# Optimization experiments

Hardware: AMD Instinct MI355X
Metric: run time of the kernel (lower is better)

The kernel has to match this reference:

```python
import jax, jax.numpy as jnp
import numpy as np

D_MODEL = 1024
NUM_HEADS = 16
NUM_KV_HEADS = 4
HEAD_DIM = D_MODEL // NUM_HEADS  # 64
KV_DIM = HEAD_DIM * NUM_KV_HEADS  # 256
B, N = 2, 2048


def setup_inputs() -> dict:
    key = jax.random.key(0)
    ks = jax.random.split(key, 7)
    std = 1.0 / np.sqrt(D_MODEL)
    return {
        "x": jax.random.normal(ks[0], (B, N, D_MODEL), dtype=jnp.float32),
        "cos": jax.random.uniform(ks[1], (N, HEAD_DIM // 2), dtype=jnp.float32),
        "sin": jax.random.uniform(ks[2], (N, HEAD_DIM // 2), dtype=jnp.float32),
        "Wq": jax.random.normal(ks[3], (D_MODEL, D_MODEL), dtype=jnp.float32) * std,
        "Wk": jax.random.normal(ks[4], (D_MODEL, KV_DIM), dtype=jnp.float32) * std,
        "Wv": jax.random.normal(ks[5], (D_MODEL, KV_DIM), dtype=jnp.float32) * std,
        "Wo": jax.random.normal(ks[6], (D_MODEL, D_MODEL), dtype=jnp.float32) * std,
    }


def _rope(t, cos, sin):
    # t: [B, H, N, head_dim]; cos/sin: [N, head_dim//2]
    t1, t2 = t[..., ::2], t[..., 1::2]
    c = cos[None, None]
    s = sin[None, None]
    # NOTE: halves are concatenated (not re-interleaved), faithful to source.
    return jnp.concatenate([t1 * c - t2 * s, t1 * s + t2 * c], axis=-1)


def reference(x, cos, sin, Wq, Wk, Wv, Wo):
    b, n, d = x.shape
    scale = HEAD_DIM ** -0.5
    q = (x @ Wq).reshape(b, n, NUM_HEADS, HEAD_DIM).transpose(0, 2, 1, 3)
    k = (x @ Wk).reshape(b, n, NUM_KV_HEADS, HEAD_DIM).transpose(0, 2, 1, 3)
    v = (x @ Wv).reshape(b, n, NUM_KV_HEADS, HEAD_DIM).transpose(0, 2, 1, 3)
    q = _rope(q, cos, sin)
    k = _rope(k, cos, sin)
    num_rep = NUM_HEADS // NUM_KV_HEADS
    k = jnp.repeat(k, num_rep, axis=1)  # [b, H, n, hd]
    v = jnp.repeat(v, num_rep, axis=1)
    attn = jnp.einsum("bhqd,bhkd->bhqk", q, k) * scale
    attn = jax.nn.softmax(attn, axis=-1)
    out = jnp.einsum("bhqk,bhkd->bhqd", attn, v)
    out = out.transpose(0, 2, 1, 3).reshape(b, n, d)
    return out @ Wo
```

## Files before the change

### kernel.cpp

```cpp
#include <hip/hip_runtime.h>
#include <math.h>

#define D_MODEL 1024
#define NHEADS  16
#define NKV     4
#define HDIM    64
#define KVDIM   256
#define BB      2
#define NN      2048
#define MROWS   (BB*NN)
#define QKVN    1536
#define NTASK   (MROWS*NHEADS)
#define NSPLIT  2
#define KVBLK   128
#define NTILE   ((NN/NSPLIT)/KVBLK)

typedef unsigned short ushort_t;
typedef unsigned int uint_t;
typedef float    f32x4 __attribute__((ext_vector_type(4)));
typedef _Float16 h16x8 __attribute__((ext_vector_type(8)));
typedef _Float16 h16x4 __attribute__((ext_vector_type(4)));
typedef __fp16   fp16x2 __attribute__((ext_vector_type(2)));

#define MFMAH(A,B,C)  __builtin_amdgcn_mfma_f32_16x16x32_f16((A),(B),(C),0,0,0)
#define MFMA16(A,B,C) __builtin_amdgcn_mfma_f32_16x16x16f16((A),(B),(C),0,0,0)
#define EXP2(x) __builtin_amdgcn_exp2f(x)

#define GLDS(gp, lp) __builtin_amdgcn_global_load_lds( \
    (const __attribute__((address_space(1))) void*)(gp), \
    (__attribute__((address_space(3))) void*)(lp), 16, 0, 0)

__device__ __forceinline__ ushort_t f2h(float f) {
    _Float16 h = (_Float16)f;
    return *(ushort_t*)&h;
}
__device__ __forceinline__ float h2f(ushort_t u) {
    return (float)(*(const _Float16*)&u);
}
__device__ __forceinline__ uint_t pk2h(float a, float b) {
    fp16x2 v = __builtin_amdgcn_cvt_pkrtz(a, b);
    return *(uint_t*)&v;
}

__global__ __launch_bounds__(256)
void prep_kernel(const float* __restrict__ x, const float* __restrict__ Wq,
                 const float* __restrict__ Wk, const float* __restrict__ Wv,
                 const float* __restrict__ Wo, ushort_t* __restrict__ xb,
                 ushort_t* __restrict__ WqkvT, ushort_t* __restrict__ WoT)
{
    __shared__ float T[32][33];
    int blk = blockIdx.x;
    if (blk < 4096) {
        const int i = blk * 256 + threadIdx.x;
        float4 v = ((const float4*)x)[i];
        uint2 o;
        o.x = pk2h(v.x, v.y);
        o.y = pk2h(v.z, v.w);
        ((uint2*)xb)[i] = o;
        return;
    }
    blk -= 4096;
    const float* src; ushort_t* dst; int N, bx, by;
    if (blk < 1024)      { src = Wq; dst = WqkvT;                            N = D_MODEL; bx = blk & 31; by = blk >> 5; }
    else if (blk < 1280) { blk -= 1024; src = Wk; dst = WqkvT + (size_t)1024 * D_MODEL; N = KVDIM; bx = blk & 7; by = blk >> 3; }
    else if (blk < 1536) { blk -= 1280; src = Wv; dst = WqkvT + (size_t)1280 * D_MODEL; N = KVDIM; bx = blk & 7; by = blk >> 3; }
    else                 { blk -= 1536; src = Wo; dst = WoT;                 N = D_MODEL; bx = blk & 31; by = blk >> 5; }
    const int tx = threadIdx.x & 31, ty = threadIdx.x >> 5;
    const int n0 = bx * 32, k0 = by * 32;
#pragma unroll
    for (int i = 0; i < 4; i++)
        T[ty + i * 8][tx] = src[(size_t)(k0 + ty + i * 8) * N + n0 + tx];
    __syncthreads();
#pragma unroll
    for (int i = 0; i < 4; i++)
        dst[(size_t)(n0 + ty + i * 8) * D_MODEL + k0 + tx] = f2h(T[tx][ty + i * 8]);
}

#define NKW (MROWS*NKV*32)
#define NKBLK (NKW / 256)
__global__ __launch_bounds__(256)
void ropevt_kernel(const ushort_t* __restrict__ QKVh, const float* __restrict__ Cos,
                   const float* __restrict__ Sin, ushort_t* __restrict__ Kb,
                   ushort_t* __restrict__ Vt)
{
    __shared__ ushort_t T[32][34];
    if (blockIdx.x >= NKBLK) {
        const int blk2 = blockIdx.x - NKBLK;
        const int bx = blk2 & 63, by = (blk2 >> 6) & 7, b = blk2 >> 9;
        const int tx = threadIdx.x & 31, ty = threadIdx.x >> 5;
        const int n0 = bx * 32, d0 = by * 32;
#pragma unroll
        for (int i = 0; i < 4; i++)
            T[ty + i * 8][tx] =
                QKVh[(size_t)(b * NN + n0 + ty + i * 8) * QKVN + 1280 + d0 + tx];
        __syncthreads();
#pragma unroll
        for (int i = 0; i < 4; i++)
            Vt[(size_t)(b * 256 + d0 + ty + i * 8) * NN + n0 + tx] = T[tx][ty + i * 8];
        return;
    }
    const int i2 = blockIdx.x * 256 + threadIdx.x;
    const int row = i2 >> 7, rem = i2 & 127;
    const int h = rem >> 5, j = rem & 31;
    const int b = row >> 11, n = row & (NN - 1);
    const uint_t pr = *(const uint_t*)&QKVh[(size_t)row * QKVN + 1024 + h * 64 + 2 * j];
    const float e = h2f((ushort_t)pr), o = h2f((ushort_t)(pr >> 16));
    const float c = Cos[n * 32 + j], s = Sin[n * 32 + j];
    ushort_t* dst = Kb + ((size_t)(b * 4 + h) * NN + n) * 64;
    dst[j]      = f2h(e * c - o * s);
    dst[j + 32] = f2h(e * s + o * c);
}

__global__ __launch_bounds__(256)
void gemm_qkv(const ushort_t* __restrict__ A, const ushort_t* __restrict__ Bt,
              ushort_t* __restrict__ C, int M, int N, int K)
{
    __shared__ ushort_t As[2][128 * 32];
    __shared__ ushort_t Bs[2][64 * 32];

    const int tid  = threadIdx.x;
    const int wave = tid >> 6, lane = tid & 63;
    const int quad = lane >> 4, l16 = lane & 15;
    const int rowBase = blockIdx.y * 128, colBase = blockIdx.x * 64;
    const int wm = (wave >> 1) * 64, wn = (wave & 1) * 32;

    f32x4 acc[4][2];
    const f32x4 zz = {0.f, 0.f, 0.f, 0.f};
#pragma unroll
    for (int i = 0; i < 4; i++)
#pragma unroll
        for (int j = 0; j < 2; j++) acc[i][j] = zz;

    const int sr = wave * 32 + (lane >> 2);
    const int sc = ((lane & 3) ^ ((lane >> 3) & 3)) * 8;
    const ushort_t* Ag0 = A + (size_t)(rowBase + sr) * K + sc;
    const ushort_t* Ag1 = A + (size_t)(rowBase + sr + 16) * K + sc;
    const int segA0 = (wave * 2 + 0) * 512, segA1 = (wave * 2 + 1) * 512;
    const int br = wave * 16 + (lane >> 2);
    const ushort_t* Bg0 = Bt + (size_t)(colBase + br) * K + sc;
    const int segB = wave * 512;

    const int fcol = (quad ^ ((l16 >> 1) & 3)) * 8;

    GLDS(Ag0, &As[0][segA0]);
    GLDS(Ag1, &As[0][segA1]);
    GLDS(Bg0, &Bs[0][segB]);

    for (int k0 = 0; k0 < K; k0 += 32) {
        const int cur = (k0 >> 5) & 1, nxt = cur ^ 1;
        __syncthreads();
        if (k0 + 32 < K) {
            GLDS(Ag0 + k0 + 32, &As[nxt][segA0]);
            GLDS(Ag1 + k0 + 32, &As[nxt][segA1]);
            GLDS(Bg0 + k0 + 32, &Bs[nxt][segB]);
        }

        h16x8 af[4], bf[2];
#pragma unroll
        for (int mt = 0; mt < 4; mt++)
            af[mt] = *(const h16x8*)&As[cur][(wm + mt * 16 + l16) * 32 + fcol];
#pragma unroll
        for (int nt = 0; nt < 2; nt++)
            bf[nt] = *(const h16x8*)&Bs[cur][(wn + nt * 16 + l16) * 32 + fcol];
#pragma unroll
        for (int mt = 0; mt < 4; mt++)
#pragma unroll
            for (int nt = 0; nt < 2; nt++)
                acc[mt][nt] = MFMAH(af[mt], bf[nt], acc[mt][nt]);
    }

#pragma unroll
    for (int mt = 0; mt < 4; mt++)
#pragma unroll
        for (int nt = 0; nt < 2; nt++) {
            const int row = rowBase + wm + mt * 16 + quad * 4;
            const int col = colBase + wn + nt * 16 + l16;
#pragma unroll
            for (int r = 0; r < 4; r++)
                C[(size_t)(row + r) * N + col] = f2h(acc[mt][nt][r]);
        }
}

__global__ __launch_bounds__(256)
void attn_mfma(const ushort_t* __restrict__ QKVh, const float* __restrict__ Cos,
               const float* __restrict__ Sin, const ushort_t* __restrict__ Kb,
               const ushort_t* __restrict__ Vt, ushort_t* __restrict__ Pnum,
               float* __restrict__ Pl)
{
    const int qt = blockIdx.x, h = blockIdx.y;
    const int b = blockIdx.z >> 1, chunk = blockIdx.z & 1;
    const int kvh = h >> 2;
    const int tid = threadIdx.x;
    const int wave = tid >> 6, lane = tid & 63;
    const int quad = lane >> 4, l16 = lane & 15;

    __shared__ ushort_t Ks[128][72];
    __shared__ ushort_t Vs[64][136];

    const int row0 = qt * 256 + wave * 64;
    const float SC = 0.125f * 1.44269504f;

    h16x8 qf[4][2];
#pragma unroll
    for (int mt = 0; mt < 4; mt++) {
        const int n = row0 + mt * 16 + l16;
        const uint_t* pr =
            (const uint_t*)(QKVh + (size_t)(b * NN + n) * QKVN + h * 64) + quad * 8;
        uint4 pa = *(const uint4*)pr;
        uint4 pc = *(const uint4*)(pr + 4);
        const uint_t pk[8] = {pa.x, pa.y, pa.z, pa.w, pc.x, pc.y, pc.z, pc.w};
        const float4 c0 = *(const float4*)&Cos[(size_t)n * 32 + quad * 8];
        const float4 c1 = *(const float4*)&Cos[(size_t)n * 32 + quad * 8 + 4];
        const float4 s0 = *(const float4*)&Sin[(size_t)n * 32 + quad * 8];
        const float4 s1 = *(const float4*)&Sin[(size_t)n * 32 + quad * 8 + 4];
        const float cc[8] = {c0.x, c0.y, c0.z, c0.w, c1.x, c1.y, c1.z, c1.w};
        const float ss[8] = {s0.x, s0.y, s0.z, s0.w, s1.x, s1.y, s1.z, s1.w};
#pragma unroll
        for (int i = 0; i < 8; i++) {
            const float e = h2f((ushort_t)pk[i]);
            const float o = h2f((ushort_t)(pk[i] >> 16));
            qf[mt][0][i] = (_Float16)((e * cc[i] - o * ss[i]) * SC);
            qf[mt][1][i] = (_Float16)((e * ss[i] + o * cc[i]) * SC);
        }
    }

    h16x4 ones;
#pragma unroll
    for (int i = 0; i < 4; i++) ones[i] = (_Float16)1.0f;

    const ushort_t* kbase = Kb + (size_t)(b * 4 + kvh) * NN * 64;
    const ushort_t* vbase = Vt + (size_t)(b * 256 + kvh * 64) * NN;
    const int key_lo = chunk * (NN / NSPLIT);
    const int rot = (qt + ((h & 3) << 2)) & (NTILE - 1);

    const int srow = tid >> 2, sseg = (tid & 3) * 8;
    const ushort_t* kp_lane = kbase + (size_t)srow * 64 + sseg;
    const ushort_t* vp_lane = vbase + (size_t)srow * NN + sseg;

    const f32x4 zz = {0.f, 0.f, 0.f, 0.f};
    f32x4 o[4][4];
#pragma unroll
    for (int mt = 0; mt < 4; mt++)
#pragma unroll
        for (int dt = 0; dt < 4; dt++) o[mt][dt] = zz;
    f32x4 lsum[4];
#pragma unroll
    for (int mt = 0; mt < 4; mt++) lsum[mt] = zz;

    const int key0 = key_lo + rot * KVBLK;
    uint4 kreg0 = *(const uint4*)(kp_lane + (size_t)key0 * 64);
    uint4 kreg1 = *(const uint4*)(kp_lane + (size_t)key0 * 64 + 32);
    uint4 kreg2 = *(const uint4*)(kp_lane + (size_t)(key0 + 64) * 64);
    uint4 kreg3 = *(const uint4*)(kp_lane + (size_t)(key0 + 64) * 64 + 32);
    uint4 vreg0 = *(const uint4*)(vp_lane + key0);
    uint4 vreg1 = *(const uint4*)(vp_lane + key0 + 32);
    uint4 vreg2 = *(const uint4*)(vp_lane + key0 + 64);
    uint4 vreg3 = *(const uint4*)(vp_lane + key0 + 96);

    for (int t = 0; t < NTILE; t++) {
        __syncthreads();
        *(uint4*)&Ks[srow][sseg]           = kreg0;
        *(uint4*)&Ks[srow][sseg + 32]      = kreg1;
        *(uint4*)&Ks[srow + 64][sseg]      = kreg2;
        *(uint4*)&Ks[srow + 64][sseg + 32] = kreg3;
        *(uint4*)&Vs[srow][sseg]           = vreg0;
        *(uint4*)&Vs[srow][sseg + 32]      = vreg1;
        *(uint4*)&Vs[srow][sseg + 64]      = vreg2;
        *(uint4*)&Vs[srow][sseg + 96]      = vreg3;
        __syncthreads();

        if (t < NTILE - 1) {
            const int kn = key_lo + ((rot + t + 1) & (NTILE - 1)) * KVBLK;
            kreg0 = *(const uint4*)(kp_lane + (size_t)kn * 64);
            kreg1 = *(const uint4*)(kp_lane + (size_t)kn * 64 + 32);
            kreg2 = *(const uint4*)(kp_lane + (size_t)(kn + 64) * 64);
            kreg3 = *(const uint4*)(kp_lane + (size_t)(kn + 64) * 64 + 32);
            vreg0 = *(const uint4*)(vp_lane + kn);
            vreg1 = *(const uint4*)(vp_lane + kn + 32);
            vreg2 = *(const uint4*)(vp_lane + kn + 64);
            vreg3 = *(const uint4*)(vp_lane + kn + 96);
        }

#pragma unroll
        for (int kt = 0; kt < 8; kt++) {
            h16x8 kf0 = *(const h16x8*)&Ks[kt * 16 + l16][quad * 8];
            h16x8 kf1 = *(const h16x8*)&Ks[kt * 16 + l16][32 + quad * 8];
            h16x4 va[4];
#pragma unroll
            for (int dt = 0; dt < 4; dt++)
                va[dt] = *(const h16x4*)&Vs[dt * 16 + l16][kt * 16 + quad * 4];

            uint2 pb[4];
#pragma unroll
            for (int mt = 0; mt < 4; mt++) {
                f32x4 st = MFMAH(kf0, qf[mt][0], zz);
                st = MFMAH(kf1, qf[mt][1], st);
                pb[mt].x = pk2h(EXP2(st[0]), EXP2(st[1]));
                pb[mt].y = pk2h(EXP2(st[2]), EXP2(st[3]));
            }
#pragma unroll
            for (int mt = 0; mt < 4; mt++) {
                const h16x4 pbv = *(const h16x4*)&pb[mt];
#pragma unroll
                for (int dt = 0; dt < 4; dt++)
                    o[mt][dt] = MFMA16(va[dt], pbv, o[mt][dt]);
                lsum[mt] = MFMA16(ones, pbv, lsum[mt]);
            }
        }
    }

    const size_t task0 = (size_t)(b * 16 + h) * NN + row0;
    ushort_t* np = Pnum + ((size_t)chunk * NTASK + task0) * 64;
#pragma unroll
    for (int mt = 0; mt < 4; mt++) {
        const float lt = lsum[mt][0];
        const float inv = 1.0f / lt;
#pragma unroll
        for (int dt = 0; dt < 4; dt++) {
            f32x4 v = o[mt][dt];
            uint2 pk;
            pk.x = pk2h(v[0] * inv, v[1] * inv);
            pk.y = pk2h(v[2] * inv, v[3] * inv);
            *(uint2*)&np[(size_t)(mt * 16 + l16) * 64 + dt * 16 + quad * 4] = pk;
        }
        if (quad == 0)
            Pl[(size_t)chunk * NTASK + task0 + mt * 16 + l16] = lt;
    }
}

__global__ __launch_bounds__(256)
void gemm_wo(const ushort_t* __restrict__ Pnum, const float* __restrict__ Pl,
             const ushort_t* __restrict__ WoT, float* __restrict__ C)
{
    __shared__ ushort_t As[2][128 * 40];
    __shared__ ushort_t Bs[2][64 * 32];

    const int tid  = threadIdx.x;
    const int wave = tid >> 6, lane = tid & 63;
    const int quad = lane >> 4, l16 = lane & 15;
    const int rowBase = blockIdx.y * 128, colBase = blockIdx.x * 64;
    const int wm = (wave >> 1) * 64, wn = (wave & 1) * 32;

    f32x4 acc[4][2];
    const f32x4 zz = {0.f, 0.f, 0.f, 0.f};
#pragma unroll
    for (int i = 0; i < 4; i++)
#pragma unroll
        for (int j = 0; j < 2; j++) acc[i][j] = zz;

    const int r0 = tid >> 2;
    const int c8 = (tid & 3) * 8;
    const int bB = rowBase >> 11;
    const int n0 = (rowBase & (NN - 1)) + r0;

    const int br = wave * 16 + (lane >> 2);
    const int sc = ((lane & 3) ^ ((lane >> 3) & 3)) * 8;
    const ushort_t* Bg0 = WoT + (size_t)(colBase + br) * D_MODEL + sc;
    const int segB = wave * 512;
    const int fcol = (quad ^ ((l16 >> 1) & 3)) * 8;

    uint4 a0c0, a0c1, a1c0, a1c1;
    float l00, l01, l10, l11;
#define PREFA(k0) { \
        const int h_ = (k0) >> 6; \
        const int d_ = ((k0) & 63) + c8; \
        const size_t t0_ = ((size_t)(bB * 16 + h_) << 11) + n0; \
        const size_t t1_ = t0_ + 64; \
        a0c0 = *(const uint4*)&Pnum[t0_ * 64 + d_]; \
        a0c1 = *(const uint4*)&Pnum[((size_t)NTASK + t0_) * 64 + d_]; \
        a1c0 = *(const uint4*)&Pnum[t1_ * 64 + d_]; \
        a1c1 = *(const uint4*)&Pnum[((size_t)NTASK + t1_) * 64 + d_]; \
        l00 = Pl[t0_]; l01 = Pl[NTASK + t0_]; \
        l10 = Pl[t1_]; l11 = Pl[NTASK + t1_]; \
    }

    PREFA(0);
    GLDS(Bg0, &Bs[0][segB]);

    for (int k0 = 0; k0 < D_MODEL; k0 += 32) {
        const int cur = (k0 >> 5) & 1, nxt = cur ^ 1;
        __syncthreads();

        {
            const float i0 = 1.f / (l00 + l01), w00 = l00 * i0, w01 = l01 * i0;
            const float i1 = 1.f / (l10 + l11), w10 = l10 * i1, w11 = l11 * i1;
            uint4 o0, o1;
            const uint_t* p0 = (const uint_t*)&a0c0;
            const uint_t* p1 = (const uint_t*)&a0c1;
            const uint_t* q0 = (const uint_t*)&a1c0;
            const uint_t* q1 = (const uint_t*)&a1c1;
            uint_t* po = (uint_t*)&o0;
            uint_t* qo = (uint_t*)&o1;
#pragma unroll
            for (int j = 0; j < 4; j++) {
                fp16x2 u = *(const fp16x2*)&p0[j];
                fp16x2 v = *(const fp16x2*)&p1[j];
                po[j] = pk2h(w00 * (float)u.x + w01 * (float)v.x,
                             w00 * (float)u.y + w01 * (float)v.y);
                fp16x2 s = *(const fp16x2*)&q0[j];
                fp16x2 r = *(const fp16x2*)&q1[j];
                qo[j] = pk2h(w10 * (float)s.x + w11 * (float)r.x,
                             w10 * (float)s.y + w11 * (float)r.y);
            }
            *(uint4*)&As[cur][r0 * 40 + c8]        = o0;
            *(uint4*)&As[cur][(r0 + 64) * 40 + c8] = o1;
        }
        __syncthreads();

        if (k0 + 32 < D_MODEL) {
            GLDS(Bg0 + k0 + 32, &Bs[nxt][segB]);
            PREFA(k0 + 32);
        }

        h16x8 af[4], bf[2];
#pragma unroll
        for (int mt = 0; mt < 4; mt++)
            af[mt] = *(const h16x8*)&As[cur][(wm + mt * 16 + l16) * 40 + quad * 8];
#pragma unroll
        for (int nt = 0; nt < 2; nt++)
            bf[nt] = *(const h16x8*)&Bs[cur][(wn + nt * 16 + l16) * 32 + fcol];
#pragma unroll
        for (int mt = 0; mt < 4; mt++)
#pragma unroll
            for (int nt = 0; nt < 2; nt++)
                acc[mt][nt] = MFMAH(af[mt], bf[nt], acc[mt][nt]);
    }
#undef PREFA

#pragma unroll
    for (int mt = 0; mt < 4; mt++)
#pragma unroll
        for (int nt = 0; nt < 2; nt++) {
            const int row = rowBase + wm + mt * 16 + quad * 4;
            const int col = colBase + wn + nt * 16 + l16;
#pragma unroll
            for (int r = 0; r < 4; r++)
                C[(size_t)(row + r) * D_MODEL + col] = acc[mt][nt][r];
        }
}

extern "C" void kernel_launch(void* const* d_in, const int* in_sizes, int n_in,
                              void* d_out, int out_size, void* d_ws, size_t ws_size,
                              hipStream_t stream)
{
    const float* x    = (const float*)d_in[0];
    const float* cosp = (const float*)d_in[1];
    const float* sinp = (const float*)d_in[2];
    const float* Wq   = (const float*)d_in[3];
    const float* Wk   = (const float*)d_in[4];
    const float* Wv   = (const float*)d_in[5];
    const float* Wo   = (const float*)d_in[6];

    char* w = (char*)d_ws;
    ushort_t* xb     = (ushort_t*)w;                       w += (size_t)MROWS * D_MODEL * 2;
    ushort_t* WqkvT  = (ushort_t*)w;                       w += (size_t)QKVN * D_MODEL * 2;
    ushort_t* WoT    = (ushort_t*)w;                       w += (size_t)D_MODEL * D_MODEL * 2;
    ushort_t* QKVh   = (ushort_t*)w;                       w += (size_t)MROWS * QKVN * 2;
    ushort_t* Kbuf   = (ushort_t*)w;                       w += (size_t)MROWS * KVDIM * 2;
    ushort_t* Vt     = (ushort_t*)w;                       w += (size_t)MROWS * KVDIM * 2;
    ushort_t* Pnum   = (ushort_t*)w;                       w += (size_t)NSPLIT * NTASK * 64 * 2;
    float*    Pl     = (float*)w;

    prep_kernel<<<6656, 256, 0, stream>>>(x, Wq, Wk, Wv, Wo, xb, WqkvT, WoT);

    gemm_qkv<<<dim3(QKVN / 64, MROWS / 128), 256, 0, stream>>>(
        xb, WqkvT, QKVh, MROWS, QKVN, D_MODEL);

    ropevt_kernel<<<NKBLK + 1024, 256, 0, stream>>>(
        QKVh, cosp, sinp, Kbuf, Vt);

    attn_mfma<<<dim3(NN / 256, NHEADS, BB * NSPLIT), 256, 0, stream>>>(
        QKVh, cosp, sinp, Kbuf, Vt, Pnum, Pl);

    gemm_wo<<<dim3(D_MODEL / 64, MROWS / 128), 256, 0, stream>>>(
        Pnum, Pl, WoT, (float*)d_out);
}
```

Before: 198.8 us.

## Split attention KV into four chunks and move combine into separate kernel

Doubles the KV split of the attention kernel from two to four chunks, so the grid has twice as many blocks and each block does half the KV tiles. The partial-result merge moves out of the output-projection GEMM into a standalone combine kernel that writes a normalized fp16 attention output buffer. The Wo GEMM then streams plain A tiles with direct global-to-LDS loads instead of combining in registers. In exchange it adds a kernel launch, doubles the partial-output traffic, and adds a full round trip through the new intermediate buffer.

Result: faster. 194.4 us (-2.2%).

```diff
diff --git a/kernel.cpp b/kernel.cpp
--- a/kernel.cpp
+++ b/kernel.cpp
@@ -11,7 +11,7 @@
 #define MROWS   (BB*NN)
 #define QKVN    1536
 #define NTASK   (MROWS*NHEADS)
-#define NSPLIT  2
+#define NSPLIT  4
 #define KVBLK   128
 #define NTILE   ((NN/NSPLIT)/KVBLK)
 
@@ -188,7 +188,7 @@
                float* __restrict__ Pl)
 {
     const int qt = blockIdx.x, h = blockIdx.y;
-    const int b = blockIdx.z >> 1, chunk = blockIdx.z & 1;
+    const int b = blockIdx.z >> 2, chunk = blockIdx.z & 3;
     const int kvh = h >> 2;
     const int tid = threadIdx.x;
     const int wave = tid >> 6, lane = tid & 63;
@@ -329,10 +329,49 @@
 }
 
 __global__ __launch_bounds__(256)
-void gemm_wo(const ushort_t* __restrict__ Pnum, const float* __restrict__ Pl,
-             const ushort_t* __restrict__ WoT, float* __restrict__ C)
-{
-    __shared__ ushort_t As[2][128 * 40];
+void combine_kernel(const ushort_t* __restrict__ Pnum, const float* __restrict__ Pl,
+                    ushort_t* __restrict__ Ob)
+{
+    const uint_t i = blockIdx.x * 256 + threadIdx.x;
+    const int row = i >> 7;
+    const int g = i & 127;
+    const int col0 = g * 8;
+    const int h = col0 >> 6, d = col0 & 63;
+    const int b = row >> 11, n = row & (NN - 1);
+    const size_t task = ((size_t)(b * 16 + h) << 11) + n;
+
+    float l[4], tot = 0.f;
+#pragma unroll
+    for (int c = 0; c < 4; c++) { l[c] = Pl[(size_t)c * NTASK + task]; tot += l[c]; }
+    const float inv = 1.f / tot;
+
+    uint4 in[4];
+#pragma unroll
+    for (int c = 0; c < 4; c++)
+        in[c] = *(const uint4*)&Pnum[((size_t)c * NTASK + task) * 64 + d];
+
+    uint4 out;
+    uint_t* po = (uint_t*)&out;
+#pragma unroll
+    for (int j = 0; j < 4; j++) {
+        float x = 0.f, y = 0.f;
+#pragma unroll
+        for (int c = 0; c < 4; c++) {
+            const float w = l[c] * inv;
+            fp16x2 u = *(const fp16x2*)&((const uint_t*)&in[c])[j];
+            x += w * (float)u.x;
+            y += w * (float)u.y;
+        }
+        po[j] = pk2h(x, y);
+    }
+    *(uint4*)&Ob[(size_t)row * D_MODEL + col0] = out;
+}
+
+__global__ __launch_bounds__(256)
+void gemm_wo(const ushort_t* __restrict__ A, const ushort_t* __restrict__ Bt,
+             float* __restrict__ C)
+{
+    __shared__ ushort_t As[2][128 * 32];
     __shared__ ushort_t Bs[2][64 * 32];
 
     const int tid  = threadIdx.x;
@@ -348,74 +387,34 @@
 #pragma unroll
         for (int j = 0; j < 2; j++) acc[i][j] = zz;
 
-    const int r0 = tid >> 2;
-    const int c8 = (tid & 3) * 8;
-    const int bB = rowBase >> 11;
-    const int n0 = (rowBase & (NN - 1)) + r0;
-
+    const int sr = wave * 32 + (lane >> 2);
+    const int sc = ((lane & 3) ^ ((lane >> 3) & 3)) * 8;
+    const ushort_t* Ag0 = A + (size_t)(rowBase + sr) * D_MODEL + sc;
+    const ushort_t* Ag1 = A + (size_t)(rowBase + sr + 16) * D_MODEL + sc;
+    const int segA0 = (wave * 2 + 0) * 512, segA1 = (wave * 2 + 1) * 512;
     const int br = wave * 16 + (lane >> 2);
-    const int sc = ((lane & 3) ^ ((lane >> 3) & 3)) * 8;
-    const ushort_t* Bg0 = WoT + (size_t)(colBase + br) * D_MODEL + sc;
+    const ushort_t* Bg0 = Bt + (size_t)(colBase + br) * D_MODEL + sc;
     const int segB = wave * 512;
+
     const int fcol = (quad ^ ((l16 >> 1) & 3)) * 8;
 
-    uint4 a0c0, a0c1, a1c0, a1c1;
-    float l00, l01, l10, l11;
-#define PREFA(k0) { \
-        const int h_ = (k0) >> 6; \
-        const int d_ = ((k0) & 63) + c8; \
-        const size_t t0_ = ((size_t)(bB * 16 + h_) << 11) + n0; \
-        const size_t t1_ = t0_ + 64; \
-        a0c0 = *(const uint4*)&Pnum[t0_ * 64 + d_]; \
-        a0c1 = *(const uint4*)&Pnum[((size_t)NTASK + t0_) * 64 + d_]; \
-        a1c0 = *(const uint4*)&Pnum[t1_ * 64 + d_]; \
-        a1c1 = *(const uint4*)&Pnum[((size_t)NTASK + t1_) * 64 + d_]; \
-        l00 = Pl[t0_]; l01 = Pl[NTASK + t0_]; \
-        l10 = Pl[t1_]; l11 = Pl[NTASK + t1_]; \
-    }
-
-    PREFA(0);
+    GLDS(Ag0, &As[0][segA0]);
+    GLDS(Ag1, &As[0][segA1]);
     GLDS(Bg0, &Bs[0][segB]);
 
     for (int k0 = 0; k0 < D_MODEL; k0 += 32) {
         const int cur = (k0 >> 5) & 1, nxt = cur ^ 1;
         __syncthreads();
-
-        {
-            const float i0 = 1.f / (l00 + l01), w00 = l00 * i0, w01 = l01 * i0;
-            const float i1 = 1.f / (l10 + l11), w10 = l10 * i1, w11 = l11 * i1;
-            uint4 o0, o1;
-            const uint_t* p0 = (const uint_t*)&a0c0;
-            const uint_t* p1 = (const uint_t*)&a0c1;
-            const uint_t* q0 = (const uint_t*)&a1c0;
-            const uint_t* q1 = (const uint_t*)&a1c1;
-            uint_t* po = (uint_t*)&o0;
-            uint_t* qo = (uint_t*)&o1;
-#pragma unroll
-            for (int j = 0; j < 4; j++) {
-                fp16x2 u = *(const fp16x2*)&p0[j];
-                fp16x2 v = *(const fp16x2*)&p1[j];
-                po[j] = pk2h(w00 * (float)u.x + w01 * (float)v.x,
-                             w00 * (float)u.y + w01 * (float)v.y);
-                fp16x2 s = *(const fp16x2*)&q0[j];
-                fp16x2 r = *(const fp16x2*)&q1[j];
-                qo[j] = pk2h(w10 * (float)s.x + w11 * (float)r.x,
-                             w10 * (float)s.y + w11 * (float)r.y);
-            }
-            *(uint4*)&As[cur][r0 * 40 + c8]        = o0;
-            *(uint4*)&As[cur][(r0 + 64) * 40 + c8] = o1;
-        }
-        __syncthreads();
-
         if (k0 + 32 < D_MODEL) {
+            GLDS(Ag0 + k0 + 32, &As[nxt][segA0]);
+            GLDS(Ag1 + k0 + 32, &As[nxt][segA1]);
             GLDS(Bg0 + k0 + 32, &Bs[nxt][segB]);
-            PREFA(k0 + 32);
         }
 
         h16x8 af[4], bf[2];
 #pragma unroll
         for (int mt = 0; mt < 4; mt++)
-            af[mt] = *(const h16x8*)&As[cur][(wm + mt * 16 + l16) * 40 + quad * 8];
+            af[mt] = *(const h16x8*)&As[cur][(wm + mt * 16 + l16) * 32 + fcol];
 #pragma unroll
         for (int nt = 0; nt < 2; nt++)
             bf[nt] = *(const h16x8*)&Bs[cur][(wn + nt * 16 + l16) * 32 + fcol];
@@ -425,7 +424,6 @@
             for (int nt = 0; nt < 2; nt++)
                 acc[mt][nt] = MFMAH(af[mt], bf[nt], acc[mt][nt]);
     }
-#undef PREFA
 
 #pragma unroll
     for (int mt = 0; mt < 4; mt++)
@@ -458,6 +456,7 @@
     ushort_t* QKVh   = (ushort_t*)w;                       w += (size_t)MROWS * QKVN * 2;
     ushort_t* Kbuf   = (ushort_t*)w;                       w += (size_t)MROWS * KVDIM * 2;
     ushort_t* Vt     = (ushort_t*)w;                       w += (size_t)MROWS * KVDIM * 2;
+    ushort_t* Obuf   = (ushort_t*)w;                       w += (size_t)MROWS * D_MODEL * 2;
     ushort_t* Pnum   = (ushort_t*)w;                       w += (size_t)NSPLIT * NTASK * 64 * 2;
     float*    Pl     = (float*)w;
 
@@ -472,6 +471,9 @@
     attn_mfma<<<dim3(NN / 256, NHEADS, BB * NSPLIT), 256, 0, stream>>>(
         QKVh, cosp, sinp, Kbuf, Vt, Pnum, Pl);
 
+    combine_kernel<<<(MROWS * D_MODEL / 8) / 256, 256, 0, stream>>>(
+        Pnum, Pl, Obuf);
+
     gemm_wo<<<dim3(D_MODEL / 64, MROWS / 128), 256, 0, stream>>>(
-        Pnum, Pl, WoT, (float*)d_out);
-}
+        Obuf, WoT, (float*)d_out);
+}
```
